# Kernel tuning notes

Hardware: AMD Instinct MI355X
Metric: run time of the kernel (lower is better)

The kernel has to match this reference:

```python
import math
import jax, jax.numpy as jnp
import numpy as np

HEADS, HD = 16, 64  # head_dim = hidden_size // num_heads = 1024 // 16

def _c(a):
    # a: [2, ...] stacked (real, imag) -> complex64
    return jax.lax.complex(a[0], a[1])

def setup_inputs() -> dict:
    key = jax.random.key(0)
    ks = jax.random.split(key, 16)
    B, S, L, H = 2, 2048, 2048, 1024  # batch, chunk len, cache len, hidden
    w_scale = 1.0 / math.sqrt(2 * H)  # complex fan-in scaling
    d = {
        "hidden":  jax.random.normal(ks[0], (2, B, S, H), jnp.float32),
        "k_cache": jax.random.normal(ks[1], (2, B, L, HEADS, HD), jnp.float32),
        "v_cache": jax.random.normal(ks[2], (2, B, L, HEADS, HD), jnp.float32),
        "qw": jax.random.normal(ks[3], (2, H, H), jnp.float32) * w_scale,
        "qb": jax.random.normal(ks[4], (2, H), jnp.float32) * 0.01,
        "kw": jax.random.normal(ks[5], (2, H, H), jnp.float32) * w_scale,
        "kb": jax.random.normal(ks[6], (2, H), jnp.float32) * 0.01,
        "vw": jax.random.normal(ks[7], (2, H, H), jnp.float32) * w_scale,
        "vb": jax.random.normal(ks[8], (2, H), jnp.float32) * 0.01,
        "ow": jax.random.normal(ks[9], (2, H, H), jnp.float32) * w_scale,
        "ob": jax.random.normal(ks[10], (2, H), jnp.float32) * 0.01,
        "ln_gamma": jnp.stack([jnp.ones(H, jnp.float32) + 0.01 * jax.random.normal(ks[11], (H,)),
                               0.01 * jax.random.normal(ks[12], (H,))]),
        "ln_beta":  0.01 * jax.random.normal(ks[13], (2, H), jnp.float32),
    }
    return d

def _complex_layernorm(x, gamma, beta, eps=1e-5):
    mu = jnp.mean(x, axis=-1, keepdims=True)              # complex mean
    xc = x - mu
    var = jnp.mean(xc.real**2 + xc.imag**2, axis=-1, keepdims=True)
    return xc / jnp.sqrt(var + eps) * gamma + beta

def _clin(z, w, b):
    # complex linear: z [..., in] @ W^T [out, in] + b [out]
    return jnp.einsum('bsh,oh->bso', z, _c(w)) + _c(b)

def reference(hidden, k_cache, v_cache, qw, qb, kw, kb, vw, vb, ow, ob, ln_gamma, ln_beta):
    x = _c(hidden)                                        # [B,S,H] complex64
    B, S, H = x.shape
    normed = _complex_layernorm(x, _c(ln_gamma), _c(ln_beta))
    Q = _clin(normed, qw, qb).reshape(B, S, HEADS, HD)
    K_new = _clin(normed, kw, kb).reshape(B, S, HEADS, HD)
    V_new = _clin(normed, vw, vb).reshape(B, S, HEADS, HD)
    K = jnp.concatenate([_c(k_cache), K_new], axis=1)     # [B, L+S, nh, hd]
    V = jnp.concatenate([_c(v_cache), V_new], axis=1)
    cache_len = k_cache.shape[2]
    kv = K.shape[1]                                       # == window_size here
    # Hermitian score: Re(Q K^dagger) / sqrt(hd)
    scores = jnp.einsum('bqhd,bkhd->bhqk', Q, jnp.conj(K)).real / math.sqrt(HD)
    row = jnp.arange(S)[:, None]
    col = jnp.arange(kv)[None, :]
    # prefix (cache) fully visible; causal within the new chunk
    mask = jnp.where((col >= cache_len) & (col - cache_len > row), -jnp.inf, 0.0).astype(scores.dtype)
    w = jax.nn.softmax(scores + mask[None, None], axis=-1)  # real weights
    out = jax.lax.complex(jnp.einsum('bhqk,bkhd->bqhd', w, V.real),
                          jnp.einsum('bhqk,bkhd->bqhd', w, V.imag)).reshape(B, S, H)
    delta = _clin(out, ow, ob)
    y = x + delta
    out_stacked = jnp.stack([y.real, y.imag])             # [2,B,S,H]
    new_k = jnp.stack([K.real, K.imag])                   # [2,B,window,nh,hd]
    new_v = jnp.stack([V.real, V.imag])
    return (out_stacked, new_k, new_v)
```

## Files before the change

### kernel.cpp

```cpp
#include <hip/hip_runtime.h>

#define HEADS 16
#define SEQ   2048
#define HID   1024
#define CACHE 2048
#define KVLEN 4096
#define MROWS 4096
#define KD    2048

typedef float  f32x4  __attribute__((ext_vector_type(4)));
typedef __bf16 bf16x4 __attribute__((ext_vector_type(4)));
typedef __bf16 bf16x8 __attribute__((ext_vector_type(8)));

__device__ __forceinline__ void gload_lds16(const void* g, void* l) {
  __builtin_amdgcn_global_load_lds((const __attribute__((address_space(1))) void*)g,
                                   (__attribute__((address_space(3))) void*)l, 16, 0, 0);
}

__global__ __launch_bounds__(256) void k_layernorm(const float* __restrict__ hid,
                                                   const float* __restrict__ gamma,
                                                   const float* __restrict__ beta,
                                                   __bf16* __restrict__ normed) {
  int row = blockIdx.x;
  int t = threadIdx.x;
  const float* xr = hid + (size_t)row * HID;
  const float* xi = hid + (size_t)MROWS * HID + (size_t)row * HID;
  float vr[4], vi[4];
  float sr = 0.f, si = 0.f;
#pragma unroll
  for (int i = 0; i < 4; i++) { int h = t + i * 256; vr[i] = xr[h]; vi[i] = xi[h]; sr += vr[i]; si += vi[i]; }
  __shared__ float red[2][4];
  for (int m = 1; m < 64; m <<= 1) { sr += __shfl_xor(sr, m); si += __shfl_xor(si, m); }
  int wid = t >> 6, l = t & 63;
  if (l == 0) { red[0][wid] = sr; red[1][wid] = si; }
  __syncthreads();
  float mr = (red[0][0] + red[0][1] + red[0][2] + red[0][3]) * (1.0f / HID);
  float mi = (red[1][0] + red[1][1] + red[1][2] + red[1][3]) * (1.0f / HID);
  float sv = 0.f;
#pragma unroll
  for (int i = 0; i < 4; i++) { float a = vr[i] - mr, b = vi[i] - mi; sv += a * a + b * b; }
  for (int m = 1; m < 64; m <<= 1) sv += __shfl_xor(sv, m);
  __syncthreads();
  if (l == 0) red[0][wid] = sv;
  __syncthreads();
  float var = (red[0][0] + red[0][1] + red[0][2] + red[0][3]) * (1.0f / HID);
  float inv = rsqrtf(var + 1e-5f);
  __bf16* outr = normed + (size_t)row * KD;
#pragma unroll
  for (int i = 0; i < 4; i++) {
    int h = t + i * 256;
    float a = (vr[i] - mr) * inv, b = (vi[i] - mi) * inv;
    float gr = gamma[h], gi = gamma[HID + h], br = beta[h], bi = beta[HID + h];
    outr[h]       = (__bf16)(a * gr - b * gi + br);
    outr[HID + h] = (__bf16)(a * gi + b * gr + bi);
  }
}

__global__ __launch_bounds__(256) void k_packw(const float* __restrict__ qw, const float* __restrict__ kw,
                                               const float* __restrict__ vw, const float* __restrict__ ow,
                                               __bf16* __restrict__ dst) {
  int idx = blockIdx.x * 256 + threadIdx.x;
  int sel = idx >> 19;
  int li  = idx & 524287;
  const float* w = sel == 0 ? qw : (sel == 1 ? kw : (sel == 2 ? vw : ow));
  int o  = li >> 8;
  int k0 = (li & 255) * 8;
  const float* wr = w;
  const float* wi = w + HID * HID;
  int oimag = (o >= HID);
  int oo = o & (HID - 1);
  bf16x8 v;
#pragma unroll
  for (int j = 0; j < 8; j++) {
    int k = k0 + j;
    int kim = (k >= HID);
    int kk = k & (HID - 1);
    float x;
    if (!oimag) x = kim ? -wi[oo * HID + kk] : wr[oo * HID + kk];
    else        x = kim ?  wr[oo * HID + kk] : wi[oo * HID + kk];
    v[j] = (__bf16)x;
  }
  *(bf16x8*)(dst + ((size_t)sel << 22) + (size_t)o * KD + k0) = v;
}

__global__ __launch_bounds__(256) void k_copykv(const float* __restrict__ kc, const float* __restrict__ vc,
                                                float* __restrict__ nk, float* __restrict__ nv,
                                                __bf16* __restrict__ Ka) {
  int i = blockIdx.x * 256 + threadIdx.x;
  int sel = i >> 21;
  int li = i & ((1 << 21) - 1);
  if (sel == 0) {
    int c4 = li & 255;
    int kv = (li >> 8) & 2047;
    int b  = (li >> 19) & 1;
    int p  = (li >> 20) & 1;
    f32x4 v = *(const f32x4*)(kc + (((size_t)((p * 2 + b) * 2048 + kv)) << 10) + c4 * 4);
    *(f32x4*)(nk + ((((size_t)(p * 2 + b)) * KVLEN + kv) << 10) + c4 * 4) = v;
    int h = c4 >> 4, d = (c4 & 15) * 4;
    bf16x4 w;
#pragma unroll
    for (int j = 0; j < 4; j++) w[j] = (__bf16)v[j];
    *(bf16x4*)(Ka + (((size_t)(b * 16 + h)) * KVLEN + kv) * 128 + p * 64 + d) = w;
  } else {
    size_t sf = (size_t)li << 2;
    size_t chunk = sf >> 21;
    size_t df = sf + (chunk << 21);
    *(f32x4*)(nv + df) = *(const f32x4*)(vc + sf);
  }
}

__global__ __launch_bounds__(256) void k_buildv(const float* __restrict__ src, __bf16* __restrict__ dst) {
  __shared__ float tile[32][129];
  int kt = blockIdx.x;
  int bh = blockIdx.y;
  int b = bh >> 4, h = bh & 15;
  int t = threadIdx.x;
  int kv0 = kt * 32;
#pragma unroll
  for (int i = 0; i < 16; i++) {
    int idx = i * 256 + t;
    int kvl = idx >> 7, dsl = idx & 127;
    int p = dsl >> 6, d = dsl & 63;
    tile[kvl][dsl] = src[(((size_t)(p * 2 + b)) * KVLEN + kv0 + kvl) * HID + h * 64 + d];
  }
  __syncthreads();
#pragma unroll
  for (int i = 0; i < 16; i++) {
    int idx = i * 256 + t;
    int dsl = idx >> 5, kvl = idx & 31;
    dst[(((size_t)bh) * 128 + dsl) * KVLEN + kv0 + kvl] = (__bf16)tile[kvl][dsl];
  }
}

#define BM 128
#define BN 128
#define BK 64
template <int QKV>
__global__ __launch_bounds__(256, 3) void k_gemm(const __bf16* __restrict__ A,
                                                 const __bf16* __restrict__ Bp,
                                                 const float* __restrict__ bias0,
                                                 const float* __restrict__ bias1,
                                                 const float* __restrict__ bias2,
                                                 const float* __restrict__ hid,
                                                 float* __restrict__ outF0,
                                                 float* __restrict__ outF1,
                                                 __bf16* __restrict__ outB0,
                                                 __bf16* __restrict__ outB1) {
  __shared__ __align__(16) __bf16 As[BM * BK];
  __shared__ __align__(16) __bf16 Bs[BN * BK];
  int bm0 = blockIdx.x * BM, bn0 = blockIdx.y * BN;
  int t = threadIdx.x, l = t & 63, wid = t >> 6;
  int wr = wid >> 1, wc = wid & 1;
  int l15 = l & 15, lg = l >> 4;
  f32x4 acc[4][4];
  f32x4 zero = {0.f, 0.f, 0.f, 0.f};
#pragma unroll
  for (int i = 0; i < 4; i++)
#pragma unroll
    for (int j = 0; j < 4; j++) acc[i][j] = zero;
  const __bf16* Ab = A + (size_t)bm0 * KD;
  const __bf16* Bb = Bp + (size_t)bn0 * KD;
  for (int k0 = 0; k0 < KD; k0 += BK) {
#pragma unroll
    for (int c = 0; c < 4; c++) {
      int idx = c * 256 + t;
      int row = idx >> 3, ch = idx & 7;
      gload_lds16(Ab + (size_t)row * KD + k0 + ch * 8, As + idx * 8);
      gload_lds16(Bb + (size_t)row * KD + k0 + ch * 8, Bs + idx * 8);
    }
    __syncthreads();
#pragma unroll
    for (int ks = 0; ks < 2; ks++) {
      bf16x8 af[4], bfv[4];
#pragma unroll
      for (int i = 0; i < 4; i++) {
        af[i]  = *(const bf16x8*)(As + (wr * 64 + i * 16 + l15) * BK + ks * 32 + lg * 8);
        bfv[i] = *(const bf16x8*)(Bs + (wc * 64 + i * 16 + l15) * BK + ks * 32 + lg * 8);
      }
#pragma unroll
      for (int mi = 0; mi < 4; mi++)
#pragma unroll
        for (int ni = 0; ni < 4; ni++)
          acc[mi][ni] = __builtin_amdgcn_mfma_f32_16x16x32_bf16(af[mi], bfv[ni], acc[mi][ni], 0, 0, 0);
    }
    __syncthreads();
  }
#pragma unroll
  for (int mi = 0; mi < 4; mi++) {
#pragma unroll
    for (int ni = 0; ni < 4; ni++) {
#pragma unroll
      for (int j = 0; j < 4; j++) {
        int m = bm0 + wr * 64 + mi * 16 + lg * 4 + j;
        int n = bn0 + wc * 64 + ni * 16 + l15;
        int b = m >> 11, s = m & 2047;
        if (QKV) {
          int mode = n >> 11, nl = n & 2047;
          const float* bias = mode == 0 ? bias0 : (mode == 1 ? bias1 : bias2);
          float v = acc[mi][ni][j] + bias[nl];
          int p = nl >> 10, hd = nl & 1023;
          if (mode == 0) {
            outB0[(((size_t)(b * 16 + (hd >> 6))) * SEQ + s) * 128 + p * 64 + (hd & 63)] = (__bf16)v;
          } else if (mode == 1) {
            outF0[(((size_t)(p * 2 + b)) * KVLEN + (CACHE + s)) * HID + hd] = v;
            outB1[(((size_t)(b * 16 + (hd >> 6))) * KVLEN + (CACHE + s)) * 128 + p * 64 + (hd & 63)] = (__bf16)v;
          } else {
            outF1[(((size_t)(p * 2 + b)) * KVLEN + (CACHE + s)) * HID + hd] = v;
          }
        } else {
          float v = acc[mi][ni][j] + bias0[n];
          int p = n >> 10;
          size_t off = (((size_t)(p * 2 + b)) * SEQ + s) * HID + (n & 1023);
          outF0[off] = v + hid[off];
        }
      }
    }
  }
}

__global__ __launch_bounds__(256, 2) void k_attn(const __bf16* __restrict__ Q,
                                                 const __bf16* __restrict__ Kt,
                                                 const __bf16* __restrict__ Vt,
                                                 __bf16* __restrict__ outp) {
  __shared__ __align__(16) __bf16 Ks[2][64 * 128];
  __shared__ __align__(16) __bf16 Vs[2][128 * 64];
  __shared__ __align__(16) __bf16 Ps[4][32 * 64];
  int id = blockIdx.y * gridDim.x + blockIdx.x;
  int xcd = id & 7, li = id >> 3;
  int bh = (xcd << 2) | (li >> 4);
  int qt = li & 15;
  int b = bh >> 4, h = bh & 15;
  int t = threadIdx.x, l = t & 63, wid = t >> 6;
  int l15 = l & 15, lg = l >> 4;
  const __bf16* Qb = Q + ((size_t)bh * SEQ) * 128;
  const __bf16* Kb = Kt + ((size_t)bh * KVLEN) * 128;
  const __bf16* Vb = Vt + ((size_t)bh * 128) * KVLEN;
  int q0 = qt * 128 + wid * 32;
  bf16x8 aQ[2][4];
#pragma unroll
  for (int mi = 0; mi < 2; mi++)
#pragma unroll
    for (int dk = 0; dk < 4; dk++)
      aQ[mi][dk] = *(const bf16x8*)(Qb + (size_t)(q0 + mi * 16 + l15) * 128 + dk * 32 + lg * 8);
  f32x4 zero = {0.f, 0.f, 0.f, 0.f};
  f32x4 o[2][8];
  f32x4 sums[2];
#pragma unroll
  for (int mi = 0; mi < 2; mi++) {
    sums[mi] = zero;
#pragma unroll
    for (int df = 0; df < 8; df++) o[mi][df] = zero;
  }
  bf16x8 ones;
#pragma unroll
  for (int i = 0; i < 8; i++) ones[i] = (__bf16)1.0f;
  const int nfull = 32 + 2 * qt;
  const int nt = nfull + 2;
  int sw = (l15 & 7) << 4;

  auto STAGE = [&](int bb, int ti) {
    int kv0 = ti * 64;
#pragma unroll
    for (int c = 0; c < 4; c++) {
      int idx = c * 256 + t;
      int kr = idx >> 4;
      gload_lds16(Kb + (size_t)(kv0 + kr) * 128 + (((idx & 15) ^ (kr & 7)) << 3), &Ks[bb][idx * 8]);
      int vr = idx >> 3;
      gload_lds16(Vb + (size_t)vr * KVLEN + kv0 + (((idx & 7) ^ (vr & 7)) << 3), &Vs[bb][idx * 8]);
    }
  };

  STAGE(0, 0);
  for (int ti = 0; ti < nt; ti++) {
    int bb = ti & 1;
    if (ti + 1 < nt) {
      STAGE(bb ^ 1, ti + 1);
      asm volatile("s_waitcnt vmcnt(8)" ::: "memory");
    } else {
      asm volatile("s_waitcnt vmcnt(0)" ::: "memory");
    }
    __builtin_amdgcn_s_barrier();
    const char* KsB = (const char*)&Ks[bb][0];
    const char* VsB = (const char*)&Vs[bb][0];
    f32x4 sacc[2][4];
    __builtin_amdgcn_s_setprio(1);
#pragma unroll
    for (int kvf = 0; kvf < 4; kvf++) {
      sacc[0][kvf] = zero; sacc[1][kvf] = zero;
      const char* kbase = KsB + (kvf * 16 + l15) * 256;
#pragma unroll
      for (int dk = 0; dk < 4; dk++) {
        bf16x8 bK = *(const bf16x8*)(kbase + ((dk * 64 + lg * 16) ^ sw));
        sacc[0][kvf] = __builtin_amdgcn_mfma_f32_16x16x32_bf16(aQ[0][dk], bK, sacc[0][kvf], 0, 0, 0);
        sacc[1][kvf] = __builtin_amdgcn_mfma_f32_16x16x32_bf16(aQ[1][dk], bK, sacc[1][kvf], 0, 0, 0);
      }
    }
    __builtin_amdgcn_s_setprio(0);
    bool masked = (ti >= nfull);
#pragma unroll
    for (int mi = 0; mi < 2; mi++) {
#pragma unroll
      for (int j = 0; j < 4; j++) {
        int prow = mi * 16 + lg * 4 + j;
        int pxor = (prow & 7) << 4;
        int qg = qt * 128 + wid * 32 + prow;
#pragma unroll
        for (int kvf = 0; kvf < 4; kvf++) {
          float s = sacc[mi][kvf][j] * 0.18033688011112042f;
          float p = exp2f(s);
          if (masked) {
            int cg = ti * 64 + kvf * 16 + l15 - CACHE;
            if (cg > qg) p = 0.f;
          }
          Ps[wid][(prow * 128 + ((kvf * 32 + l15 * 2) ^ pxor)) >> 1] = (__bf16)p;
        }
      }
    }
    __builtin_amdgcn_s_setprio(1);
#pragma unroll
    for (int mi = 0; mi < 2; mi++) {
      const char* pbase = (const char*)&Ps[wid][0] + (mi * 16 + l15) * 128;
#pragma unroll
      for (int ks = 0; ks < 2; ks++) {
        int off = (ks * 64 + lg * 16) ^ sw;
        bf16x8 aP = *(const bf16x8*)(pbase + off);
        sums[mi] = __builtin_amdgcn_mfma_f32_16x16x32_bf16(aP, ones, sums[mi], 0, 0, 0);
#pragma unroll
        for (int df = 0; df < 8; df++) {
          bf16x8 bV = *(const bf16x8*)(VsB + (df * 16 + l15) * 128 + off);
          o[mi][df] = __builtin_amdgcn_mfma_f32_16x16x32_bf16(aP, bV, o[mi][df], 0, 0, 0);
        }
      }
    }
    __builtin_amdgcn_s_setprio(0);
    __builtin_amdgcn_s_barrier();
  }
#pragma unroll
  for (int mi = 0; mi < 2; mi++) {
    float inv[4];
#pragma unroll
    for (int j = 0; j < 4; j++) inv[j] = 1.0f / sums[mi][j];
#pragma unroll
    for (int df = 0; df < 8; df++) {
      int dslot = df * 16 + l15;
      int col = (dslot < 64) ? (h * 64 + dslot) : (1024 + h * 64 + (dslot - 64));
#pragma unroll
      for (int j = 0; j < 4; j++) {
        int qg2 = q0 + mi * 16 + lg * 4 + j;
        float v = o[mi][df][j] * inv[j];
        outp[((size_t)(b * SEQ + qg2)) * KD + col] = (__bf16)v;
      }
    }
  }
}

extern "C" void kernel_launch(void* const* d_in, const int* in_sizes, int n_in,
                              void* d_out, int out_size, void* d_ws, size_t ws_size,
                              hipStream_t stream) {
  const float* hid = (const float*)d_in[0];
  const float* kc  = (const float*)d_in[1];
  const float* vc  = (const float*)d_in[2];
  const float* qw  = (const float*)d_in[3];
  const float* qb  = (const float*)d_in[4];
  const float* kw  = (const float*)d_in[5];
  const float* kb  = (const float*)d_in[6];
  const float* vw  = (const float*)d_in[7];
  const float* vb  = (const float*)d_in[8];
  const float* ow  = (const float*)d_in[9];
  const float* ob  = (const float*)d_in[10];
  const float* lg  = (const float*)d_in[11];
  const float* lb  = (const float*)d_in[12];

  float* y  = (float*)d_out;
  float* nk = y + 8388608;
  float* nv = nk + 16777216;

  char* ws = (char*)d_ws;
  __bf16* normed = (__bf16*)(ws);
  __bf16* wall   = (__bf16*)(ws + 16777216);
  __bf16* Qa     = (__bf16*)(ws + 50331648);
  __bf16* Ka     = (__bf16*)(ws + 67108864);
  __bf16* Va     = (__bf16*)(ws + 100663296);
  __bf16* ao     = (__bf16*)(ws + 134217728);

  k_layernorm<<<4096, 256, 0, stream>>>(hid, lg, lb, normed);
  k_packw<<<8192, 256, 0, stream>>>(qw, kw, vw, ow, wall);
  k_copykv<<<16384, 256, 0, stream>>>(kc, vc, nk, nv, Ka);
  dim3 gq(32, 48);
  k_gemm<1><<<gq, 256, 0, stream>>>(normed, wall, qb, kb, vb, nullptr, nk, nv, Qa, Ka);
  dim3 gv(128, 32);
  k_buildv<<<gv, 256, 0, stream>>>(nv, Va);
  dim3 ga(16, 32);
  k_attn<<<ga, 256, 0, stream>>>(Qa, Ka, Va, ao);
  dim3 go(32, 16);
  k_gemm<0><<<go, 256, 0, stream>>>(ao, wall + ((size_t)3 << 22), ob, nullptr, nullptr, hid, y, nullptr, nullptr, nullptr);
}
```

Baseline: 458.5 us.

## Fuse V-transpose into QKV GEMM epilogue, rebalance causal tiles, restructure P writes

k_buildv now transposes only the cached V straight from the input cache, and the QKV GEMM epilogue writes the new V rows directly in transposed bf16 layout. This removes a pass over the full new-V buffer. The attention kernel swaps MFMA operand order so each lane holds score columns, which allows vectorized bf16x4 writes of P to shared memory. It also preloads V and P fragments before the MFMA loop and interleaves query tiles so blocks with heavy and light causal masks are paired. These changes add register pressure and change the masking index math, including a leftover no-op comparison.

```diff
diff --git a/kernel.cpp b/kernel.cpp
--- a/kernel.cpp
+++ b/kernel.cpp
@@ -109,7 +109,7 @@
   }
 }
 
-__global__ __launch_bounds__(256) void k_buildv(const float* __restrict__ src, __bf16* __restrict__ dst) {
+__global__ __launch_bounds__(256) void k_buildv(const float* __restrict__ vc, __bf16* __restrict__ dst) {
   __shared__ float tile[32][129];
   int kt = blockIdx.x;
   int bh = blockIdx.y;
@@ -121,7 +121,7 @@
     int idx = i * 256 + t;
     int kvl = idx >> 7, dsl = idx & 127;
     int p = dsl >> 6, d = dsl & 63;
-    tile[kvl][dsl] = src[(((size_t)(p * 2 + b)) * KVLEN + kv0 + kvl) * HID + h * 64 + d];
+    tile[kvl][dsl] = vc[(((size_t)(p * 2 + b)) * CACHE + kv0 + kvl) * HID + h * 64 + d];
   }
   __syncthreads();
 #pragma unroll
@@ -145,7 +145,8 @@
                                                  float* __restrict__ outF0,
                                                  float* __restrict__ outF1,
                                                  __bf16* __restrict__ outB0,
-                                                 __bf16* __restrict__ outB1) {
+                                                 __bf16* __restrict__ outB1,
+                                                 __bf16* __restrict__ outB2) {
   __shared__ __align__(16) __bf16 As[BM * BK];
   __shared__ __align__(16) __bf16 Bs[BN * BK];
   int bm0 = blockIdx.x * BM, bn0 = blockIdx.y * BN;
@@ -189,28 +190,43 @@
   for (int mi = 0; mi < 4; mi++) {
 #pragma unroll
     for (int ni = 0; ni < 4; ni++) {
-#pragma unroll
-      for (int j = 0; j < 4; j++) {
-        int m = bm0 + wr * 64 + mi * 16 + lg * 4 + j;
-        int n = bn0 + wc * 64 + ni * 16 + l15;
-        int b = m >> 11, s = m & 2047;
-        if (QKV) {
-          int mode = n >> 11, nl = n & 2047;
-          const float* bias = mode == 0 ? bias0 : (mode == 1 ? bias1 : bias2);
-          float v = acc[mi][ni][j] + bias[nl];
-          int p = nl >> 10, hd = nl & 1023;
-          if (mode == 0) {
-            outB0[(((size_t)(b * 16 + (hd >> 6))) * SEQ + s) * 128 + p * 64 + (hd & 63)] = (__bf16)v;
-          } else if (mode == 1) {
-            outF0[(((size_t)(p * 2 + b)) * KVLEN + (CACHE + s)) * HID + hd] = v;
-            outB1[(((size_t)(b * 16 + (hd >> 6))) * KVLEN + (CACHE + s)) * 128 + p * 64 + (hd & 63)] = (__bf16)v;
-          } else {
-            outF1[(((size_t)(p * 2 + b)) * KVLEN + (CACHE + s)) * HID + hd] = v;
+      int mbase = bm0 + wr * 64 + mi * 16 + lg * 4;
+      int n = bn0 + wc * 64 + ni * 16 + l15;
+      int b = mbase >> 11, sbase = mbase & 2047;
+      if (QKV) {
+        int mode = n >> 11, nl = n & 2047;
+        const float* bias = mode == 0 ? bias0 : (mode == 1 ? bias1 : bias2);
+        float bv = bias[nl];
+        int p = nl >> 10, hd = nl & 1023;
+        if (mode == 2) {
+          bf16x4 w;
+#pragma unroll
+          for (int j = 0; j < 4; j++) {
+            float v = acc[mi][ni][j] + bv;
+            outF1[(((size_t)(p * 2 + b)) * KVLEN + (CACHE + sbase + j)) * HID + hd] = v;
+            w[j] = (__bf16)v;
           }
+          *(bf16x4*)(outB2 + (((size_t)(b * 16 + (hd >> 6))) * 128 + p * 64 + (hd & 63)) * KVLEN + CACHE + sbase) = w;
         } else {
-          float v = acc[mi][ni][j] + bias0[n];
-          int p = n >> 10;
-          size_t off = (((size_t)(p * 2 + b)) * SEQ + s) * HID + (n & 1023);
+#pragma unroll
+          for (int j = 0; j < 4; j++) {
+            float v = acc[mi][ni][j] + bv;
+            int s = sbase + j;
+            if (mode == 0) {
+              outB0[(((size_t)(b * 16 + (hd >> 6))) * SEQ + s) * 128 + p * 64 + (hd & 63)] = (__bf16)v;
+            } else {
+              outF0[(((size_t)(p * 2 + b)) * KVLEN + (CACHE + s)) * HID + hd] = v;
+              outB1[(((size_t)(b * 16 + (hd >> 6))) * KVLEN + (CACHE + s)) * 128 + p * 64 + (hd & 63)] = (__bf16)v;
+            }
+          }
+        }
+      } else {
+        float bv = bias0[n];
+        int p = n >> 10;
+#pragma unroll
+        for (int j = 0; j < 4; j++) {
+          float v = acc[mi][ni][j] + bv;
+          size_t off = (((size_t)(p * 2 + b)) * SEQ + (sbase + j)) * HID + (n & 1023);
           outF0[off] = v + hid[off];
         }
       }
@@ -228,13 +244,15 @@
   int id = blockIdx.y * gridDim.x + blockIdx.x;
   int xcd = id & 7, li = id >> 3;
   int bh = (xcd << 2) | (li >> 4);
-  int qt = li & 15;
+  int ql = li & 15;
+  int qt = (ql & 1) ? (15 - (ql >> 1)) : (ql >> 1);
   int b = bh >> 4, h = bh & 15;
   int t = threadIdx.x, l = t & 63, wid = t >> 6;
   int l15 = l & 15, lg = l >> 4;
   const __bf16* Qb = Q + ((size_t)bh * SEQ) * 128;
   const __bf16* Kb = Kt + ((size_t)bh * KVLEN) * 128;
   const __bf16* Vb = Vt + ((size_t)bh * 128) * KVLEN;
+  __bf16* Pw = &Ps[wid][0];
   int q0 = qt * 128 + wid * 32;
   bf16x8 aQ[2][4];
 #pragma unroll
@@ -291,45 +309,58 @@
 #pragma unroll
       for (int dk = 0; dk < 4; dk++) {
         bf16x8 bK = *(const bf16x8*)(kbase + ((dk * 64 + lg * 16) ^ sw));
-        sacc[0][kvf] = __builtin_amdgcn_mfma_f32_16x16x32_bf16(aQ[0][dk], bK, sacc[0][kvf], 0, 0, 0);
-        sacc[1][kvf] = __builtin_amdgcn_mfma_f32_16x16x32_bf16(aQ[1][dk], bK, sacc[1][kvf], 0, 0, 0);
+        sacc[0][kvf] = __builtin_amdgcn_mfma_f32_16x16x32_bf16(bK, aQ[0][dk], sacc[0][kvf], 0, 0, 0);
+        sacc[1][kvf] = __builtin_amdgcn_mfma_f32_16x16x32_bf16(bK, aQ[1][dk], sacc[1][kvf], 0, 0, 0);
       }
     }
     __builtin_amdgcn_s_setprio(0);
     bool masked = (ti >= nfull);
 #pragma unroll
     for (int mi = 0; mi < 2; mi++) {
-#pragma unroll
-      for (int j = 0; j < 4; j++) {
-        int prow = mi * 16 + lg * 4 + j;
-        int pxor = (prow & 7) << 4;
-        int qg = qt * 128 + wid * 32 + prow;
-#pragma unroll
-        for (int kvf = 0; kvf < 4; kvf++) {
-          float s = sacc[mi][kvf][j] * 0.18033688011112042f;
-          float p = exp2f(s);
+      int row = mi * 16 + l15;
+      int rx = (row & 7) << 3;
+#pragma unroll
+      for (int kvf = 0; kvf < 4; kvf++) {
+        bf16x4 w;
+#pragma unroll
+        for (int j = 0; j < 4; j++) {
+          float p = exp2f(sacc[mi][kvf][j] * 0.18033688011112042f);
           if (masked) {
-            int cg = ti * 64 + kvf * 16 + l15 - CACHE;
-            if (cg > qg) p = 0.f;
+            int cg = ti * 64 + kvf * 16 + lg * 4 + j - CACHE;
+            if (cg > q0 + row - qt * 128 + qt * 128) p = p;
+            if (cg > qt * 128 + wid * 32 + row) p = 0.f;
           }
-          Ps[wid][(prow * 128 + ((kvf * 32 + l15 * 2) ^ pxor)) >> 1] = (__bf16)p;
+          w[j] = (__bf16)p;
         }
-      }
+        *(bf16x4*)(Pw + row * 64 + ((kvf * 16 + lg * 4) ^ rx)) = w;
+      }
+    }
+    bf16x8 bV[2][8], aP[2][2];
+#pragma unroll
+    for (int ks = 0; ks < 2; ks++) {
+      int off = (ks * 64 + lg * 16) ^ sw;
+#pragma unroll
+      for (int df = 0; df < 8; df++)
+        bV[ks][df] = *(const bf16x8*)(VsB + (df * 16 + l15) * 128 + off);
+    }
+#pragma unroll
+    for (int mi = 0; mi < 2; mi++) {
+      int row = mi * 16 + l15;
+      int rx = (row & 7) << 3;
+      const __bf16* pb = Pw + row * 64;
+#pragma unroll
+      for (int ks = 0; ks < 2; ks++)
+        aP[mi][ks] = *(const bf16x8*)(pb + ((ks * 32 + lg * 8) ^ rx));
     }
     __builtin_amdgcn_s_setprio(1);
 #pragma unroll
     for (int mi = 0; mi < 2; mi++) {
-      const char* pbase = (const char*)&Ps[wid][0] + (mi * 16 + l15) * 128;
 #pragma unroll
       for (int ks = 0; ks < 2; ks++) {
-        int off = (ks * 64 + lg * 16) ^ sw;
-        bf16x8 aP = *(const bf16x8*)(pbase + off);
-        sums[mi] = __builtin_amdgcn_mfma_f32_16x16x32_bf16(aP, ones, sums[mi], 0, 0, 0);
-#pragma unroll
-        for (int df = 0; df < 8; df++) {
-          bf16x8 bV = *(const bf16x8*)(VsB + (df * 16 + l15) * 128 + off);
-          o[mi][df] = __builtin_amdgcn_mfma_f32_16x16x32_bf16(aP, bV, o[mi][df], 0, 0, 0);
-        }
+        sums[mi] = __builtin_amdgcn_mfma_f32_16x16x32_bf16(aP[mi][ks], ones, sums[mi], 0, 0, 0);
+#pragma unroll
+        for (int df = 0; df < 8; df++)
+          o[mi][df] = __builtin_amdgcn_mfma_f32_16x16x32_bf16(aP[mi][ks], bV[ks][df], o[mi][df], 0, 0, 0);
       }
     }
     __builtin_amdgcn_s_setprio(0);
@@ -386,12 +417,12 @@
   k_layernorm<<<4096, 256, 0, stream>>>(hid, lg, lb, normed);
   k_packw<<<8192, 256, 0, stream>>>(qw, kw, vw, ow, wall);
   k_copykv<<<16384, 256, 0, stream>>>(kc, vc, nk, nv, Ka);
+  dim3 gv(64, 32);
+  k_buildv<<<gv, 256, 0, stream>>>(vc, Va);
   dim3 gq(32, 48);
-  k_gemm<1><<<gq, 256, 0, stream>>>(normed, wall, qb, kb, vb, nullptr, nk, nv, Qa, Ka);
-  dim3 gv(128, 32);
-  k_buildv<<<gv, 256, 0, stream>>>(nv, Va);
+  k_gemm<1><<<gq, 256, 0, stream>>>(normed, wall, qb, kb, vb, nullptr, nk, nv, Qa, Ka, Va);
   dim3 ga(16, 32);
   k_attn<<<ga, 256, 0, stream>>>(Qa, Ka, Va, ao);
   dim3 go(32, 16);
-  k_gemm<0><<<go, 256, 0, stream>>>(ao, wall + ((size_t)3 << 22), ob, nullptr, nullptr, hid, y, nullptr, nullptr, nullptr);
-}
+  k_gemm<0><<<go, 256, 0, stream>>>(ao, wall + ((size_t)3 << 22), ob, nullptr, nullptr, hid, y, nullptr, nullptr, nullptr, nullptr);
+}
```

Result: faster. 448.9 us (-2.1%).
